# Performance work log

Measured on AMD Instinct MI355X. Metric: run time of the kernel, lower is better.

Reference implementation:

```python
import jax, jax.numpy as jnp
import numpy as np

N = 8192
TD, ID, D = 768, 1024, 1024
E = 8
GH = D // 2  # gate hidden
EPS = 1e-5


def _init_linear(key, fan_in, shape):
    # torch nn.Linear default init: U(-1/sqrt(fan_in), 1/sqrt(fan_in))
    bound = 1.0 / np.sqrt(fan_in)
    return jax.random.uniform(key, shape, jnp.float32, -bound, bound)


def setup_inputs() -> dict:
    key = jax.random.key(0)
    ks = jax.random.split(key, 16)
    return {
        "text_features": jax.random.normal(ks[0], (N, TD), jnp.float32),
        "image_features": jax.random.normal(ks[1], (N, ID), jnp.float32),
        "Wt": _init_linear(ks[2], TD, (TD, D)),
        "bt": _init_linear(ks[3], TD, (D,)),
        "Wi": _init_linear(ks[4], ID, (ID, D)),
        "bi": _init_linear(ks[5], ID, (D,)),
        "eW1": _init_linear(ks[6], 2 * D, (E, 2 * D, D)),
        "eb1": _init_linear(ks[7], 2 * D, (E, D)),
        "eW2": _init_linear(ks[8], D, (E, D, D)),
        "eb2": _init_linear(ks[9], D, (E, D)),
        "ln_g": jnp.ones((E, D), jnp.float32),
        "ln_b": jnp.zeros((E, D), jnp.float32),
        "gW1": _init_linear(ks[10], 2 * D, (2 * D, GH)),
        "gb1": _init_linear(ks[11], 2 * D, (GH,)),
        "gW2": _init_linear(ks[12], GH, (GH, E)),
        "gb2": _init_linear(ks[13], GH, (E,)),
    }


def reference(text_features, image_features, Wt, bt, Wi, bi,
              eW1, eb1, eW2, eb2, ln_g, ln_b, gW1, gb1, gW2, gb2):
    # project both modalities to shared dim D (dropout is identity in eval)
    ta = text_features @ Wt + bt            # [N, D]
    ia = image_features @ Wi + bi           # [N, D]
    c = jnp.concatenate([ta, ia], axis=-1)  # [N, 2D]

    # gating MLP -> softmax over experts
    gh = jax.nn.silu(c @ gW1 + gb1)                      # [N, GH]
    w = jax.nn.softmax(gh @ gW2 + gb2, axis=-1)          # [N, E]

    # all experts densely, batched over E
    h = jax.nn.silu(jnp.einsum('nc,ecd->ned', c, eW1) + eb1)   # [N, E, D]
    o = jnp.einsum('ned,edf->nef', h, eW2) + eb2               # [N, E, D]

    # per-expert LayerNorm over last dim
    mu = o.mean(axis=-1, keepdims=True)
    var = ((o - mu) ** 2).mean(axis=-1, keepdims=True)
    o = (o - mu) * jax.lax.rsqrt(var + EPS) * ln_g + ln_b      # [N, E, D]

    # gate-weighted sum over experts
    return jnp.einsum('ned,ne->nd', o, w)                      # [N, D]
```

## Files before the change

kernel.cpp:

```cpp
#include <hip/hip_runtime.h>

#define NROWS 8192
#define TDIM 768
#define IDIM 1024
#define DDIM 1024
#define NEXP 8
#define GHID 512

typedef __attribute__((ext_vector_type(8))) short short8;
typedef __attribute__((ext_vector_type(4))) float f4;
typedef __attribute__((ext_vector_type(4))) unsigned short us4;

__device__ __forceinline__ unsigned short f2bf(float f) {
  union { float f; unsigned u; } v; v.f = f;
  unsigned r = v.u + 0x7FFF + ((v.u >> 16) & 1);
  return (unsigned short)(r >> 16);
}
__device__ __forceinline__ float bf2f(unsigned short u) {
  union { unsigned u; float f; } v; v.u = ((unsigned)u) << 16;
  return v.f;
}

__device__ __forceinline__ void gload16(const void* g, void* l) {
  __builtin_amdgcn_global_load_lds(
      (const __attribute__((address_space(1))) void*)g,
      (__attribute__((address_space(3))) void*)l, 16, 0, 0);
}

__global__ __launch_bounds__(256) void cast_bf16_kernel(
    const float* __restrict__ src, unsigned short* __restrict__ dst, int n4) {
  int i = blockIdx.x * 256 + threadIdx.x;
  if (i < n4) {
    f4 v = ((const f4*)src)[i];
    us4 o;
    o[0] = f2bf(v[0]); o[1] = f2bf(v[1]); o[2] = f2bf(v[2]); o[3] = f2bf(v[3]);
    ((us4*)dst)[i] = o;
  }
}

__global__ __launch_bounds__(256) void transpose_cast_kernel(
    const float* __restrict__ src, unsigned short* __restrict__ dst, int R, int C) {
  __shared__ float tile[64][65];
  size_t base = (size_t)blockIdx.z * R * C;
  int c0 = blockIdx.x * 64, r0 = blockIdx.y * 64;
  int tx = threadIdx.x & 63, ty = threadIdx.x >> 6;
#pragma unroll
  for (int j = 0; j < 64; j += 4)
    tile[ty + j][tx] = src[base + (size_t)(r0 + ty + j) * C + c0 + tx];
  __syncthreads();
  const int tid = threadIdx.x;
#pragma unroll
  for (int i = 0; i < 2; i++) {
    int row = i * 32 + (tid >> 3);
    int c8 = (tid & 7) * 8;
    short8 v;
#pragma unroll
    for (int u = 0; u < 8; u++) v[u] = (short)f2bf(tile[c8 + u][row]);
    *(short8*)&dst[base + (size_t)(c0 + row) * R + r0 + c8] = v;
  }
}

template <int SILU, int OUTBF, int COLMAJ>
__global__ __launch_bounds__(512, 1) void gemm256_kernel(
    const unsigned short* __restrict__ A, const unsigned short* __restrict__ BT,
    const float* __restrict__ bias, void* __restrict__ Cptr,
    int K, int lda, int ldb, int ldc,
    size_t sA, size_t sB, size_t sBias, size_t sC) {
  __shared__ __align__(16) char LDS[131072];

  const unsigned short* Ab = A + (size_t)blockIdx.z * sA;
  const unsigned short* Bb = BT + (size_t)blockIdx.z * sB;
  const float* biasb = bias + (size_t)blockIdx.z * sBias;

  const int gx = gridDim.x, gy = gridDim.y;
  const int nwg = gx * gy;
  const int orig = blockIdx.y * gx + blockIdx.x;
  const int q = nwg >> 3, r = nwg & 7;
  const int xcd = orig & 7, idx = orig >> 3;
  const int wgid = (xcd < r ? xcd * (q + 1) : r * (q + 1) + (xcd - r) * q) + idx;
  const int bx = COLMAJ ? (wgid / gy) : (wgid % gx);
  const int by = COLMAJ ? (wgid % gy) : (wgid / gx);

  const int tid = threadIdx.x;
  const int wave = tid >> 6, lane = tid & 63;
  const int wm = wave >> 2, wn = wave & 3;
  const int row0 = by * 256, col0 = bx * 256;

  f4 acc[8][4] = {};

  const int srow = tid >> 3;
  const int scolg = ((tid & 7) << 4) ^ (((tid >> 3) & 7) << 4);
  const size_t lda2 = (size_t)lda * 2, ldb2 = (size_t)ldb * 2;
  const char* Abytes = (const char*)Ab;
  const char* Bbytes = (const char*)Bb;
  const size_t aG = (size_t)(row0 + srow) * lda2 + scolg;
  const size_t bG = (size_t)(col0 + srow) * ldb2 + scolg;
  char* ldsw = LDS + wave * 1024;

  auto stageA0 = [&](int tt) {
    const size_t kb = (size_t)tt << 7;
    char* d = ldsw + ((tt & 1) << 16);
    gload16(Abytes + aG + kb, d);
    gload16(Abytes + aG + (size_t)64 * lda2 + kb, d + 8192);
  };
  auto stageA1 = [&](int tt) {
    const size_t kb = (size_t)tt << 7;
    char* d = ldsw + ((tt & 1) << 16);
    gload16(Abytes + aG + (size_t)128 * lda2 + kb, d + 16384);
    gload16(Abytes + aG + (size_t)192 * lda2 + kb, d + 24576);
  };
  auto stageB0 = [&](int tt) {
    const size_t kb = (size_t)tt << 7;
    char* d = ldsw + ((tt & 1) << 16) + 32768;
    gload16(Bbytes + bG + kb, d);
    gload16(Bbytes + bG + (size_t)64 * ldb2 + kb, d + 8192);
  };
  auto stageB1 = [&](int tt) {
    const size_t kb = (size_t)tt << 7;
    char* d = ldsw + ((tt & 1) << 16) + 32768;
    gload16(Bbytes + bG + (size_t)128 * ldb2 + kb, d + 16384);
    gload16(Bbytes + bG + (size_t)192 * ldb2 + kb, d + 24576);
  };

  const int aBase = (wm * 128 + (lane & 15)) * 128;
  const int bBase = 32768 + (wn * 64 + (lane & 15)) * 128;
  const int ck0 = ((lane >> 4) << 4) ^ ((lane & 7) << 4);

  const int NT = K >> 6;

  stageA0(0); stageA1(0); stageB0(0); stageB1(0);
  if (NT > 1) { stageB0(1); stageB1(1); }
  asm volatile("s_waitcnt vmcnt(4)" ::: "memory");
  __builtin_amdgcn_s_barrier();

  short8 bv[4][2];
  for (int t = 0; t < NT; t++) {
    const int aB = ((t & 1) << 16) + aBase;
    const int bB = ((t & 1) << 16) + bBase;

    {
      short8 av[2][2];
#pragma unroll
      for (int n = 0; n < 4; n++)
#pragma unroll
        for (int kk = 0; kk < 2; kk++)
          bv[n][kk] = *(const short8*)(LDS + bB + n * 2048 + (ck0 ^ (kk << 6)));
#pragma unroll
      for (int m = 0; m < 2; m++)
#pragma unroll
        for (int kk = 0; kk < 2; kk++)
          av[m][kk] = *(const short8*)(LDS + aB + m * 2048 + (ck0 ^ (kk << 6)));
      if (t + 1 < NT) stageA0(t + 1);
      asm volatile("s_waitcnt lgkmcnt(8)" ::: "memory");
      __builtin_amdgcn_sched_barrier(0);
      __builtin_amdgcn_s_barrier();
      asm volatile("s_waitcnt lgkmcnt(0)" ::: "memory");
      __builtin_amdgcn_sched_barrier(0);
      __builtin_amdgcn_s_setprio(1);
#pragma unroll
      for (int kk = 0; kk < 2; kk++)
#pragma unroll
        for (int m = 0; m < 2; m++)
#pragma unroll
          for (int n = 0; n < 4; n++)
            acc[m][n] = __builtin_amdgcn_mfma_f32_16x16x32_bf16(av[m][kk], bv[n][kk], acc[m][n], 0, 0, 0);
      __builtin_amdgcn_s_setprio(0);
      __builtin_amdgcn_s_barrier();
    }

#pragma unroll
    for (int ph = 1; ph < 4; ph++) {
      short8 av[2][2];
#pragma unroll
      for (int m = 0; m < 2; m++)
#pragma unroll
        for (int kk = 0; kk < 2; kk++)
          av[m][kk] = *(const short8*)(LDS + aB + (ph * 2 + m) * 2048 + (ck0 ^ (kk << 6)));
      if (ph == 1) {
        if (t + 1 < NT) stageA1(t + 1);
      } else if (ph == 2) {
        if (t + 2 < NT) stageB0(t + 2);
      } else {
        if (t + 2 < NT) stageB1(t + 2);
      }
      __builtin_amdgcn_sched_barrier(0);
      __builtin_amdgcn_s_barrier();
      asm volatile("s_waitcnt lgkmcnt(0)" ::: "memory");
      __builtin_amdgcn_sched_barrier(0);
      __builtin_amdgcn_s_setprio(1);
#pragma unroll
      for (int kk = 0; kk < 2; kk++)
#pragma unroll
        for (int m = 0; m < 2; m++)
#pragma unroll
          for (int n = 0; n < 4; n++)
            acc[ph * 2 + m][n] = __builtin_amdgcn_mfma_f32_16x16x32_bf16(av[m][kk], bv[n][kk], acc[ph * 2 + m][n], 0, 0, 0);
      __builtin_amdgcn_s_setprio(0);
      if (ph == 3) {
        if (t + 2 < NT) {
          asm volatile("s_waitcnt vmcnt(4)" ::: "memory");
        } else if (t + 1 < NT) {
          asm volatile("s_waitcnt vmcnt(0)" ::: "memory");
        }
      }
      __builtin_amdgcn_s_barrier();
    }
  }

  const int crow0 = row0 + wm * 128 + (lane >> 4) * 4;
  const int ccol0 = col0 + wn * 64 + (lane & 15);
  char* Cb = (char*)Cptr + (size_t)blockIdx.z * sC * (OUTBF ? 2 : 4);
  float bvv[4];
#pragma unroll
  for (int n = 0; n < 4; n++) bvv[n] = biasb[ccol0 + n * 16];
#pragma unroll
  for (int m = 0; m < 8; m++) {
#pragma unroll
    for (int r2 = 0; r2 < 4; r2++) {
      const size_t rowb = (size_t)(crow0 + m * 16 + r2) * ldc;
#pragma unroll
      for (int n = 0; n < 4; n++) {
        float v = acc[m][n][r2] + bvv[n];
        if (SILU) v = v / (1.0f + __expf(-v));
        const size_t cidx = rowb + ccol0 + n * 16;
        if (OUTBF) ((unsigned short*)Cb)[cidx] = f2bf(v);
        else       ((float*)Cb)[cidx] = v;
      }
    }
  }
}

template <int SILU, int OUTBF>
__global__ __launch_bounds__(256) void gemm_tn_kernel(
    const unsigned short* __restrict__ A, const unsigned short* __restrict__ BT,
    const float* __restrict__ bias, void* __restrict__ Cptr,
    int K, int lda, int ldb, int ldc,
    size_t sA, size_t sB, size_t sBias, size_t sC) {
  __shared__ unsigned short Als[128 * 32];
  __shared__ unsigned short Bls[128 * 32];

  const unsigned short* Ab = A + (size_t)blockIdx.z * sA;
  const unsigned short* Bb = BT + (size_t)blockIdx.z * sB;
  const float* biasb = bias + (size_t)blockIdx.z * sBias;

  const int gx = gridDim.x;
  const int nwg = gx * gridDim.y;
  const int orig = blockIdx.y * gx + blockIdx.x;
  const int q = nwg >> 3, r = nwg & 7;
  const int xcd = orig & 7, idx = orig >> 3;
  const int wgid = (xcd < r ? xcd * (q + 1) : r * (q + 1) + (xcd - r) * q) + idx;
  const int bx = wgid % gx, by = wgid / gx;

  const int tid = threadIdx.x;
  const int wave = tid >> 6, lane = tid & 63;
  const int row0 = by * 128, col0 = bx * 128;
  const int wm = wave >> 1, wn = wave & 1;
  f4 acc[4][4] = {};

  const int aoff = (wm * 64 + (lane & 15)) * 32 + (lane >> 4) * 8;
  const int boff = (wn * 64 + (lane & 15)) * 32 + (lane >> 4) * 8;

  const int L0 = tid, L1 = tid + 256;
  const size_t aofs0 = (size_t)(row0 + (L0 >> 2)) * lda + (L0 & 3) * 8;
  const size_t aofs1 = (size_t)(row0 + (L1 >> 2)) * lda + (L1 & 3) * 8;
  const size_t bofs0 = (size_t)(col0 + (L0 >> 2)) * ldb + (L0 & 3) * 8;
  const size_t bofs1 = (size_t)(col0 + (L1 >> 2)) * ldb + (L1 & 3) * 8;
  char* abase0 = (char*)Als + wave * 1024;
  char* abase1 = (char*)Als + 4096 + wave * 1024;
  char* bbase0 = (char*)Bls + wave * 1024;
  char* bbase1 = (char*)Bls + 4096 + wave * 1024;

  for (int k0 = 0; k0 < K; k0 += 32) {
    gload16(Ab + aofs0 + k0, abase0);
    gload16(Ab + aofs1 + k0, abase1);
    gload16(Bb + bofs0 + k0, bbase0);
    gload16(Bb + bofs1 + k0, bbase1);
    __syncthreads();
    short8 af[4], bfr[4];
#pragma unroll
    for (int i = 0; i < 4; i++) af[i] = *(const short8*)&Als[aoff + i * 512];
#pragma unroll
    for (int j = 0; j < 4; j++) bfr[j] = *(const short8*)&Bls[boff + j * 512];
#pragma unroll
    for (int i = 0; i < 4; i++)
#pragma unroll
      for (int j = 0; j < 4; j++)
        acc[i][j] = __builtin_amdgcn_mfma_f32_16x16x32_bf16(af[i], bfr[j], acc[i][j], 0, 0, 0);
    __syncthreads();
  }

  const int crow = row0 + wm * 64 + (lane >> 4) * 4;
  const int ccol = col0 + wn * 64 + (lane & 15);
  char* Cb = (char*)Cptr + (size_t)blockIdx.z * sC * (OUTBF ? 2 : 4);
  float bvv[4];
#pragma unroll
  for (int j = 0; j < 4; j++) bvv[j] = biasb[ccol + j * 16];
#pragma unroll
  for (int i = 0; i < 4; i++) {
#pragma unroll
    for (int r2 = 0; r2 < 4; r2++) {
      const size_t rowb = (size_t)(crow + i * 16 + r2) * ldc;
#pragma unroll
      for (int j = 0; j < 4; j++) {
        float v = acc[i][j][r2] + bvv[j];
        if (SILU) v = v / (1.0f + __expf(-v));
        const size_t cidx = rowb + ccol + j * 16;
        if (OUTBF)
          ((unsigned short*)Cb)[cidx] = f2bf(v);
        else
          ((float*)Cb)[cidx] = v;
      }
    }
  }
}

__global__ __launch_bounds__(256) void proj2_kernel(
    const unsigned short* __restrict__ A0, const unsigned short* __restrict__ A1,
    const unsigned short* __restrict__ B0, const unsigned short* __restrict__ B1,
    const float* __restrict__ bias0, const float* __restrict__ bias1,
    unsigned short* __restrict__ Cptr) {
  __shared__ unsigned short Als[128 * 32];
  __shared__ unsigned short Bls[128 * 32];

  const int z = blockIdx.z;
  const unsigned short* Ab = z ? A1 : A0;
  const unsigned short* Bb = z ? B1 : B0;
  const float* biasb = z ? bias1 : bias0;
  const int K = z ? IDIM : TDIM;
  const int ldc = 2 * DDIM;

  const int gx = gridDim.x;
  const int nwg = gx * gridDim.y;
  const int orig = blockIdx.y * gx + blockIdx.x;
  const int q = nwg >> 3, r = nwg & 7;
  const int xcd = orig & 7, idx = orig >> 3;
  const int wgid = (xcd < r ? xcd * (q + 1) : r * (q + 1) + (xcd - r) * q) + idx;
  const int bx = wgid % gx, by = wgid / gx;

  const int tid = threadIdx.x;
  const int wave = tid >> 6, lane = tid & 63;
  const int row0 = by * 128, col0 = bx * 128;
  const int wm = wave >> 1, wn = wave & 1;
  f4 acc[4][4] = {};

  const int aoff = (wm * 64 + (lane & 15)) * 32 + (lane >> 4) * 8;
  const int boff = (wn * 64 + (lane & 15)) * 32 + (lane >> 4) * 8;

  const int L0 = tid, L1 = tid + 256;
  const size_t aofs0 = (size_t)(row0 + (L0 >> 2)) * K + (L0 & 3) * 8;
  const size_t aofs1 = (size_t)(row0 + (L1 >> 2)) * K + (L1 & 3) * 8;
  const size_t bofs0 = (size_t)(col0 + (L0 >> 2)) * K + (L0 & 3) * 8;
  const size_t bofs1 = (size_t)(col0 + (L1 >> 2)) * K + (L1 & 3) * 8;
  char* abase0 = (char*)Als + wave * 1024;
  char* abase1 = (char*)Als + 4096 + wave * 1024;
  char* bbase0 = (char*)Bls + wave * 1024;
  char* bbase1 = (char*)Bls + 4096 + wave * 1024;

  for (int k0 = 0; k0 < K; k0 += 32) {
    gload16(Ab + aofs0 + k0, abase0);
    gload16(Ab + aofs1 + k0, abase1);
    gload16(Bb + bofs0 + k0, bbase0);
    gload16(Bb + bofs1 + k0, bbase1);
    __syncthreads();
    short8 af[4], bfr[4];
#pragma unroll
    for (int i = 0; i < 4; i++) af[i] = *(const short8*)&Als[aoff + i * 512];
#pragma unroll
    for (int j = 0; j < 4; j++) bfr[j] = *(const short8*)&Bls[boff + j * 512];
#pragma unroll
    for (int i = 0; i < 4; i++)
#pragma unroll
      for (int j = 0; j < 4; j++)
        acc[i][j] = __builtin_amdgcn_mfma_f32_16x16x32_bf16(af[i], bfr[j], acc[i][j], 0, 0, 0);
    __syncthreads();
  }

  const int crow = row0 + wm * 64 + (lane >> 4) * 4;
  const int ccolL = col0 + wn * 64 + (lane & 15);
  const int ccol = z * DDIM + ccolL;
  float bvv[4];
#pragma unroll
  for (int j = 0; j < 4; j++) bvv[j] = biasb[ccolL + j * 16];
#pragma unroll
  for (int i = 0; i < 4; i++) {
#pragma unroll
    for (int r2 = 0; r2 < 4; r2++) {
      const size_t rowb = (size_t)(crow + i * 16 + r2) * ldc;
#pragma unroll
      for (int j = 0; j < 4; j++) {
        float v = acc[i][j][r2] + bvv[j];
        Cptr[rowb + ccol + j * 16] = f2bf(v);
      }
    }
  }
}

__global__ __launch_bounds__(256) void gate_kernel(
    const unsigned short* __restrict__ gh, const float* __restrict__ gW2,
    const float* __restrict__ gb2, float* __restrict__ wout) {
  __shared__ float sW[NEXP * GHID];
  int tid = threadIdx.x;
  for (int i = tid; i < GHID * NEXP; i += 256) {
    int k = i >> 3, e = i & 7;
    sW[e * GHID + k] = gW2[i];
  }
  __syncthreads();
  int wave = tid >> 6, lane = tid & 63;
  int row = blockIdx.x * 4 + wave;
  float acc[NEXP] = {};
#pragma unroll
  for (int i = 0; i < 8; i++) {
    int k = lane + 64 * i;
    float x = bf2f(gh[(size_t)row * GHID + k]);
#pragma unroll
    for (int e = 0; e < NEXP; e++) acc[e] += x * sW[e * GHID + k];
  }
#pragma unroll
  for (int off = 32; off; off >>= 1)
#pragma unroll
    for (int e = 0; e < NEXP; e++) acc[e] += __shfl_xor(acc[e], off);
  float lg[NEXP], mx = -1e30f;
#pragma unroll
  for (int e = 0; e < NEXP; e++) { lg[e] = acc[e] + gb2[e]; mx = fmaxf(mx, lg[e]); }
  float s = 0.f;
#pragma unroll
  for (int e = 0; e < NEXP; e++) { lg[e] = __expf(lg[e] - mx); s += lg[e]; }
  if (lane < NEXP) wout[(size_t)row * NEXP + lane] = lg[lane] / s;
}

__global__ __launch_bounds__(256) void ln_acc8_kernel(
    const unsigned short* __restrict__ o, const float* __restrict__ wgate,
    const float* __restrict__ ln_g, const float* __restrict__ ln_b,
    float* __restrict__ out, int row0) {
  int wave = threadIdx.x >> 6, lane = threadIdx.x & 63;
  int lrow = blockIdx.x * 4 + wave;
  int grow = row0 + lrow;
  float res[16];
#pragma unroll
  for (int u = 0; u < 16; u++) res[u] = 0.f;
#pragma unroll
  for (int e = 0; e < NEXP; e++) {
    const unsigned short* orow = o + (size_t)lrow * (NEXP * DDIM) + (size_t)e * DDIM;
    float xs[16];
    float s = 0.f, s2 = 0.f;
#pragma unroll
    for (int qq = 0; qq < 2; qq++) {
      short8 t = *(const short8*)&orow[qq * 512 + lane * 8];
#pragma unroll
      for (int u = 0; u < 8; u++) {
        float x = bf2f((unsigned short)t[u]);
        xs[qq * 8 + u] = x;
        s += x;
        s2 += x * x;
      }
    }
#pragma unroll
    for (int off = 32; off; off >>= 1) {
      s += __shfl_xor(s, off);
      s2 += __shfl_xor(s2, off);
    }
    const float inv = 1.0f / 1024.0f;
    float mu = s * inv;
    float var = s2 * inv - mu * mu;
    float rr = rsqrtf(var + 1e-5f);
    float wv = wgate[(size_t)grow * NEXP + e];
#pragma unroll
    for (int qq = 0; qq < 2; qq++) {
      int d = qq * 512 + lane * 8;
#pragma unroll
      for (int u = 0; u < 8; u++) {
        float gg = ln_g[(size_t)e * DDIM + d + u];
        float bb = ln_b[(size_t)e * DDIM + d + u];
        res[qq * 8 + u] += wv * ((xs[qq * 8 + u] - mu) * rr * gg + bb);
      }
    }
  }
  size_t rowbase = (size_t)grow * DDIM;
#pragma unroll
  for (int qq = 0; qq < 2; qq++) {
#pragma unroll
    for (int h = 0; h < 2; h++) {
      f4 t;
#pragma unroll
      for (int u = 0; u < 4; u++) t[u] = res[qq * 8 + h * 4 + u];
      *(f4*)&out[rowbase + qq * 512 + lane * 8 + h * 4] = t;
    }
  }
}

extern "C" void kernel_launch(void* const* d_in, const int* in_sizes, int n_in,
                              void* d_out, int out_size, void* d_ws, size_t ws_size,
                              hipStream_t stream) {
  const float* text  = (const float*)d_in[0];
  const float* image = (const float*)d_in[1];
  const float* Wt    = (const float*)d_in[2];
  const float* bt    = (const float*)d_in[3];
  const float* Wi    = (const float*)d_in[4];
  const float* bi    = (const float*)d_in[5];
  const float* eW1   = (const float*)d_in[6];
  const float* eb1   = (const float*)d_in[7];
  const float* eW2   = (const float*)d_in[8];
  const float* eb2   = (const float*)d_in[9];
  const float* ln_g  = (const float*)d_in[10];
  const float* ln_b  = (const float*)d_in[11];
  const float* gW1   = (const float*)d_in[12];
  const float* gb1   = (const float*)d_in[13];
  const float* gW2   = (const float*)d_in[14];
  const float* gb2   = (const float*)d_in[15];
  float* out = (float*)d_out;

  size_t off = 0;
  auto alloc = [&](size_t bytes) -> void* {
    void* p = (char*)d_ws + off;
    off += (bytes + 255) & ~(size_t)255;
    return p;
  };
  unsigned short* eW1T = (unsigned short*)alloc((size_t)NEXP * 2 * DDIM * DDIM * 2);
  unsigned short* eW2T = (unsigned short*)alloc((size_t)NEXP * DDIM * DDIM * 2);
  unsigned short* c_bf = (unsigned short*)alloc((size_t)NROWS * 2 * DDIM * 2);
  float* wgate         = (float*)alloc((size_t)NROWS * NEXP * 4);
  const size_t overlay0 = off;

  unsigned short* text_bf = (unsigned short*)alloc((size_t)NROWS * TDIM * 2);
  unsigned short* img_bf  = (unsigned short*)alloc((size_t)NROWS * IDIM * 2);
  unsigned short* WtT     = (unsigned short*)alloc((size_t)TDIM * DDIM * 2);
  unsigned short* WiT     = (unsigned short*)alloc((size_t)IDIM * DDIM * 2);
  unsigned short* gW1T    = (unsigned short*)alloc((size_t)2 * DDIM * GHID * 2);
  unsigned short* gh_bf   = (unsigned short*)alloc((size_t)NROWS * GHID * 2);

  int slab = 8192;
  while (slab > 256 &&
         overlay0 + (size_t)slab * (size_t)(2 * NEXP * DDIM + 2 * NEXP * DDIM) > ws_size)
    slab >>= 1;
  unsigned short* h_slab = (unsigned short*)((char*)d_ws + overlay0);
  unsigned short* o_slab = (unsigned short*)((char*)d_ws + overlay0 +
                                             (size_t)slab * NEXP * DDIM * 2);

  cast_bf16_kernel<<<(NROWS * TDIM / 4 + 255) / 256, 256, 0, stream>>>(text, text_bf, NROWS * TDIM / 4);
  cast_bf16_kernel<<<(NROWS * IDIM / 4 + 255) / 256, 256, 0, stream>>>(image, img_bf, NROWS * IDIM / 4);

  transpose_cast_kernel<<<dim3(DDIM / 64, TDIM / 64, 1), 256, 0, stream>>>(Wt, WtT, TDIM, DDIM);
  transpose_cast_kernel<<<dim3(DDIM / 64, IDIM / 64, 1), 256, 0, stream>>>(Wi, WiT, IDIM, DDIM);
  transpose_cast_kernel<<<dim3(GHID / 64, 2 * DDIM / 64, 1), 256, 0, stream>>>(gW1, gW1T, 2 * DDIM, GHID);
  transpose_cast_kernel<<<dim3(DDIM / 64, 2 * DDIM / 64, NEXP), 256, 0, stream>>>(eW1, eW1T, 2 * DDIM, DDIM);
  transpose_cast_kernel<<<dim3(DDIM / 64, DDIM / 64, NEXP), 256, 0, stream>>>(eW2, eW2T, DDIM, DDIM);

  proj2_kernel<<<dim3(DDIM / 128, NROWS / 128, 2), 256, 0, stream>>>(
      text_bf, img_bf, WtT, WiT, bt, bi, c_bf);

  gemm_tn_kernel<1, 1><<<dim3(GHID / 128, NROWS / 128), 256, 0, stream>>>(
      c_bf, gW1T, gb1, gh_bf, 2 * DDIM, 2 * DDIM, 2 * DDIM, GHID, 0, 0, 0, 0);

  gate_kernel<<<NROWS / 4, 256, 0, stream>>>(gh_bf, gW2, gb2, wgate);

  for (int r0 = 0; r0 < NROWS; r0 += slab) {
    gemm256_kernel<1, 1, 1><<<dim3(NEXP * DDIM / 256, slab / 256), 512, 0, stream>>>(
        c_bf + (size_t)r0 * 2 * DDIM, eW1T, eb1, h_slab,
        2 * DDIM, 2 * DDIM, 2 * DDIM, NEXP * DDIM, 0, 0, 0, 0);
    gemm256_kernel<0, 1, 0><<<dim3(DDIM / 256, slab / 256, NEXP), 512, 0, stream>>>(
        h_slab, eW2T, eb2, o_slab,
        DDIM, NEXP * DDIM, DDIM, NEXP * DDIM,
        (size_t)DDIM, (size_t)DDIM * DDIM, (size_t)DDIM, (size_t)DDIM);
    ln_acc8_kernel<<<slab / 4, 256, 0, stream>>>(o_slab, wgate, ln_g, ln_b, out, r0);
  }
}
```

Before: 663.7 us.

## Shrink GEMM K-tile to 32 with simpler two-phase double-buffered pipeline

Halves the per-iteration K depth of the 256x256 GEMM from 64 to 32, cutting the LDS footprint from 128KB to 64KB. The four-phase schedule that prefetched B two tiles ahead is replaced by a two-phase loop that prefetches A and B only one tile ahead and waits for all outstanding loads each iteration. This simplifies the pipeline and frees LDS, but doubles the number of barriers per unit of K and reduces how far global loads can run ahead of the MFMAs.

```diff
diff --git a/kernel.cpp b/kernel.cpp
--- a/kernel.cpp
+++ b/kernel.cpp
@@ -66,7 +66,7 @@
     const float* __restrict__ bias, void* __restrict__ Cptr,
     int K, int lda, int ldb, int ldc,
     size_t sA, size_t sB, size_t sBias, size_t sC) {
-  __shared__ __align__(16) char LDS[131072];
+  __shared__ __align__(16) char LDS[65536];
 
   const unsigned short* Ab = A + (size_t)blockIdx.z * sA;
   const unsigned short* Bb = BT + (size_t)blockIdx.z * sB;
@@ -88,8 +88,8 @@
 
   f4 acc[8][4] = {};
 
-  const int srow = tid >> 3;
-  const int scolg = ((tid & 7) << 4) ^ (((tid >> 3) & 7) << 4);
+  const int srow = tid >> 2;
+  const int scolg = ((tid & 3) << 4) ^ (((tid >> 2) & 3) << 4);
   const size_t lda2 = (size_t)lda * 2, ldb2 = (size_t)ldb * 2;
   const char* Abytes = (const char*)Ab;
   const char* Bbytes = (const char*)Bb;
@@ -97,111 +97,75 @@
   const size_t bG = (size_t)(col0 + srow) * ldb2 + scolg;
   char* ldsw = LDS + wave * 1024;
 
-  auto stageA0 = [&](int tt) {
-    const size_t kb = (size_t)tt << 7;
-    char* d = ldsw + ((tt & 1) << 16);
+  auto stageA = [&](int tt) {
+    const size_t kb = (size_t)tt << 6;
+    char* d = ldsw + ((tt & 1) << 15);
     gload16(Abytes + aG + kb, d);
-    gload16(Abytes + aG + (size_t)64 * lda2 + kb, d + 8192);
+    gload16(Abytes + aG + (size_t)128 * lda2 + kb, d + 8192);
   };
-  auto stageA1 = [&](int tt) {
-    const size_t kb = (size_t)tt << 7;
-    char* d = ldsw + ((tt & 1) << 16);
-    gload16(Abytes + aG + (size_t)128 * lda2 + kb, d + 16384);
-    gload16(Abytes + aG + (size_t)192 * lda2 + kb, d + 24576);
+  auto stageB = [&](int tt) {
+    const size_t kb = (size_t)tt << 6;
+    char* d = ldsw + ((tt & 1) << 15) + 16384;
+    gload16(Bbytes + bG + kb, d);
+    gload16(Bbytes + bG + (size_t)128 * ldb2 + kb, d + 8192);
   };
-  auto stageB0 = [&](int tt) {
-    const size_t kb = (size_t)tt << 7;
-    char* d = ldsw + ((tt & 1) << 16) + 32768;
-    gload16(Bbytes + bG + kb, d);
-    gload16(Bbytes + bG + (size_t)64 * ldb2 + kb, d + 8192);
-  };
-  auto stageB1 = [&](int tt) {
-    const size_t kb = (size_t)tt << 7;
-    char* d = ldsw + ((tt & 1) << 16) + 32768;
-    gload16(Bbytes + bG + (size_t)128 * ldb2 + kb, d + 16384);
-    gload16(Bbytes + bG + (size_t)192 * ldb2 + kb, d + 24576);
-  };
-
-  const int aBase = (wm * 128 + (lane & 15)) * 128;
-  const int bBase = 32768 + (wn * 64 + (lane & 15)) * 128;
-  const int ck0 = ((lane >> 4) << 4) ^ ((lane & 7) << 4);
-
-  const int NT = K >> 6;
-
-  stageA0(0); stageA1(0); stageB0(0); stageB1(0);
-  if (NT > 1) { stageB0(1); stageB1(1); }
-  asm volatile("s_waitcnt vmcnt(4)" ::: "memory");
+
+  const int aBase = (wm * 128 + (lane & 15)) * 64;
+  const int bBase = 16384 + (wn * 64 + (lane & 15)) * 64;
+  const int ck0 = ((lane >> 4) << 4) ^ ((lane & 3) << 4);
+
+  const int NT = K >> 5;
+
+  stageA(0); stageB(0);
+  asm volatile("s_waitcnt vmcnt(0)" ::: "memory");
   __builtin_amdgcn_s_barrier();
 
-  short8 bv[4][2];
   for (int t = 0; t < NT; t++) {
-    const int aB = ((t & 1) << 16) + aBase;
-    const int bB = ((t & 1) << 16) + bBase;
-
+    const int buf = (t & 1) << 15;
+
+    short8 bv[4];
     {
-      short8 av[2][2];
+      short8 av[4];
 #pragma unroll
       for (int n = 0; n < 4; n++)
-#pragma unroll
-        for (int kk = 0; kk < 2; kk++)
-          bv[n][kk] = *(const short8*)(LDS + bB + n * 2048 + (ck0 ^ (kk << 6)));
-#pragma unroll
-      for (int m = 0; m < 2; m++)
-#pragma unroll
-        for (int kk = 0; kk < 2; kk++)
-          av[m][kk] = *(const short8*)(LDS + aB + m * 2048 + (ck0 ^ (kk << 6)));
-      if (t + 1 < NT) stageA0(t + 1);
-      asm volatile("s_waitcnt lgkmcnt(8)" ::: "memory");
+        bv[n] = *(const short8*)(LDS + buf + bBase + n * 1024 + ck0);
+#pragma unroll
+      for (int m = 0; m < 4; m++)
+        av[m] = *(const short8*)(LDS + buf + aBase + m * 1024 + ck0);
+      if (t + 1 < NT) stageA(t + 1);
       __builtin_amdgcn_sched_barrier(0);
       __builtin_amdgcn_s_barrier();
       asm volatile("s_waitcnt lgkmcnt(0)" ::: "memory");
       __builtin_amdgcn_sched_barrier(0);
       __builtin_amdgcn_s_setprio(1);
 #pragma unroll
-      for (int kk = 0; kk < 2; kk++)
-#pragma unroll
-        for (int m = 0; m < 2; m++)
-#pragma unroll
-          for (int n = 0; n < 4; n++)
-            acc[m][n] = __builtin_amdgcn_mfma_f32_16x16x32_bf16(av[m][kk], bv[n][kk], acc[m][n], 0, 0, 0);
+      for (int m = 0; m < 4; m++)
+#pragma unroll
+        for (int n = 0; n < 4; n++)
+          acc[m][n] = __builtin_amdgcn_mfma_f32_16x16x32_bf16(av[m], bv[n], acc[m][n], 0, 0, 0);
       __builtin_amdgcn_s_setprio(0);
       __builtin_amdgcn_s_barrier();
     }
 
-#pragma unroll
-    for (int ph = 1; ph < 4; ph++) {
-      short8 av[2][2];
-#pragma unroll
-      for (int m = 0; m < 2; m++)
-#pragma unroll
-        for (int kk = 0; kk < 2; kk++)
-          av[m][kk] = *(const short8*)(LDS + aB + (ph * 2 + m) * 2048 + (ck0 ^ (kk << 6)));
-      if (ph == 1) {
-        if (t + 1 < NT) stageA1(t + 1);
-      } else if (ph == 2) {
-        if (t + 2 < NT) stageB0(t + 2);
-      } else {
-        if (t + 2 < NT) stageB1(t + 2);
-      }
+    {
+      short8 av[4];
+#pragma unroll
+      for (int m = 0; m < 4; m++)
+        av[m] = *(const short8*)(LDS + buf + aBase + (4 + m) * 1024 + ck0);
+      if (t + 1 < NT) stageB(t + 1);
       __builtin_amdgcn_sched_barrier(0);
       __builtin_amdgcn_s_barrier();
       asm volatile("s_waitcnt lgkmcnt(0)" ::: "memory");
       __builtin_amdgcn_sched_barrier(0);
       __builtin_amdgcn_s_setprio(1);
 #pragma unroll
-      for (int kk = 0; kk < 2; kk++)
-#pragma unroll
-        for (int m = 0; m < 2; m++)
-#pragma unroll
-          for (int n = 0; n < 4; n++)
-            acc[ph * 2 + m][n] = __builtin_amdgcn_mfma_f32_16x16x32_bf16(av[m][kk], bv[n][kk], acc[ph * 2 + m][n], 0, 0, 0);
+      for (int m = 0; m < 4; m++)
+#pragma unroll
+        for (int n = 0; n < 4; n++)
+          acc[4 + m][n] = __builtin_amdgcn_mfma_f32_16x16x32_bf16(av[m], bv[n], acc[4 + m][n], 0, 0, 0);
       __builtin_amdgcn_s_setprio(0);
-      if (ph == 3) {
-        if (t + 2 < NT) {
-          asm volatile("s_waitcnt vmcnt(4)" ::: "memory");
-        } else if (t + 1 < NT) {
-          asm volatile("s_waitcnt vmcnt(0)" ::: "memory");
-        }
+      if (t + 1 < NT) {
+        asm volatile("s_waitcnt vmcnt(0)" ::: "memory");
       }
       __builtin_amdgcn_s_barrier();
     }
```

Result: slower. 700.0 us (+5.5%).
